# Kernel tuning notes

Hardware: AMD Instinct MI355X
Metric: run time of the kernel (lower is better)

## Reference

```python
import jax, jax.numpy as jnp
import numpy as np

PROJ_DIM = 8192
INPUT_DIM = 512
THRESH = 1e-08


def _signed_sqrt(x):
    return jnp.sign(x) * jnp.sqrt(jnp.abs(x))


def _make_sketch_matrix(key, input_dim, proj_dim):
    kh, ks = jax.random.split(key)
    h = jax.random.randint(kh, (input_dim,), 0, proj_dim)
    s = jnp.sign(jax.random.uniform(ks, (input_dim,), minval=-1.0, maxval=1.0)).astype(jnp.float32)
    M = jnp.zeros((input_dim, proj_dim), dtype=jnp.float32)
    return M.at[jnp.arange(input_dim), h].set(s)


def setup_inputs() -> dict:
    key = jax.random.key(0)
    kx, k1, k2 = jax.random.split(key, 3)
    x = jax.random.normal(kx, (32, 14, 14, INPUT_DIM), dtype=jnp.float32)
    M1 = _make_sketch_matrix(k1, INPUT_DIM, PROJ_DIM)
    M2 = _make_sketch_matrix(k2, INPUT_DIM, PROJ_DIM)
    return {"x": x, "M1": M1, "M2": M2}


def reference(x, M1, M2):
    B, H, W, C = x.shape
    x_flat = x.reshape(-1, C)                      # [B*H*W, C]
    # count-sketch projections (dense matmul, as in the original layer)
    p1 = (x_flat @ M1).astype(jnp.complex64)       # [B*H*W, P]
    p2 = (x_flat @ M2).astype(jnp.complex64)
    # circular convolution via FFT
    sketch = jnp.fft.fft(p1, axis=-1) * jnp.fft.fft(p2, axis=-1)
    y = jnp.real(jnp.fft.ifft(sketch, axis=-1)).astype(jnp.float32)
    y = y.reshape(B, H, W, -1).sum(axis=(1, 2))    # sum-pool over spatial dims -> [B, P]
    y = _signed_sqrt(y)
    # tf.nn.l2_normalize(x, axis=1, epsilon=1e-10)
    inv_norm = jax.lax.rsqrt(jnp.maximum(jnp.sum(y * y, axis=1, keepdims=True), 1e-10))
    return y * inv_norm
```

## Files before the change

### kernel.cpp

```cpp
#include <hip/hip_runtime.h>
#include <math.h>

#define PROJ 8192
#define CDIM 512
#define HWPOS 196
#define NBATCH 32
#define SPLITS 32
#define ROWS_PER_SPLIT (CDIM / SPLITS)

__global__ __launch_bounds__(256) void extract_kernel(
    const float* __restrict__ M1, const float* __restrict__ M2,
    int* __restrict__ h1, float* __restrict__ s1,
    int* __restrict__ h2, float* __restrict__ s2,
    float* __restrict__ norm)
{
    const int row = blockIdx.x;
    const float* M = blockIdx.y ? M2 : M1;
    int*   h = blockIdx.y ? h2 : h1;
    float* s = blockIdx.y ? s2 : s1;
    const float* mrow = M + (size_t)row * PROJ;

    if (blockIdx.x == 0 && blockIdx.y == 0 && threadIdx.x < NBATCH)
        norm[threadIdx.x] = 0.0f;

    for (int i = threadIdx.x * 4; i < PROJ; i += 256 * 4) {
        float4 v = *(const float4*)(mrow + i);
        if (v.x != 0.0f) { h[row] = i + 0; s[row] = v.x; }
        if (v.y != 0.0f) { h[row] = i + 1; s[row] = v.y; }
        if (v.z != 0.0f) { h[row] = i + 2; s[row] = v.z; }
        if (v.w != 0.0f) { h[row] = i + 3; s[row] = v.w; }
    }
}

__global__ __launch_bounds__(256) void gram_kernel(
    const float* __restrict__ x, float* __restrict__ G)
{
    const int bat = blockIdx.z;
    const int bi  = blockIdx.x;
    const int bj  = blockIdx.y;

    __shared__ __align__(16) float As[8][128];
    __shared__ __align__(16) float Bs[8][128];

    const float* Xb = x + (size_t)bat * HWPOS * CDIM;

    float acc[8][8];
#pragma unroll
    for (int i = 0; i < 8; ++i)
#pragma unroll
        for (int j = 0; j < 8; ++j) acc[i][j] = 0.0f;

    const int tid  = threadIdx.x;
    const int ti   = tid >> 4;
    const int tj   = tid & 15;
    const int lrow = tid >> 5;
    const int lcol = (tid & 31) * 4;

    for (int k0 = 0; k0 < HWPOS; k0 += 8) {
        const int krow = k0 + lrow;
        float4 a4 = make_float4(0.f, 0.f, 0.f, 0.f);
        float4 b4 = make_float4(0.f, 0.f, 0.f, 0.f);
        if (krow < HWPOS) {
            const float* xr = Xb + (size_t)krow * CDIM;
            a4 = *(const float4*)(xr + bi * 128 + lcol);
            b4 = *(const float4*)(xr + bj * 128 + lcol);
        }
        *(float4*)&As[lrow][lcol] = a4;
        *(float4*)&Bs[lrow][lcol] = b4;
        __syncthreads();

#pragma unroll
        for (int kk = 0; kk < 8; ++kk) {
            float4 alo = *(const float4*)&As[kk][ti * 8];
            float4 ahi = *(const float4*)&As[kk][ti * 8 + 4];
            float4 blo = *(const float4*)&Bs[kk][tj * 8];
            float4 bhi = *(const float4*)&Bs[kk][tj * 8 + 4];
            float av[8] = {alo.x, alo.y, alo.z, alo.w, ahi.x, ahi.y, ahi.z, ahi.w};
            float bv[8] = {blo.x, blo.y, blo.z, blo.w, bhi.x, bhi.y, bhi.z, bhi.w};
#pragma unroll
            for (int i = 0; i < 8; ++i)
#pragma unroll
                for (int j = 0; j < 8; ++j)
                    acc[i][j] = fmaf(av[i], bv[j], acc[i][j]);
        }
        __syncthreads();
    }

    float* Gb = G + (size_t)bat * CDIM * CDIM;
#pragma unroll
    for (int i = 0; i < 8; ++i) {
        const int row = bi * 128 + ti * 8 + i;
        float* gr = Gb + (size_t)row * CDIM + bj * 128 + tj * 8;
        *(float4*)(gr)     = make_float4(acc[i][0], acc[i][1], acc[i][2], acc[i][3]);
        *(float4*)(gr + 4) = make_float4(acc[i][4], acc[i][5], acc[i][6], acc[i][7]);
    }
}

__global__ __launch_bounds__(256) void scatter_partial_kernel(
    float* __restrict__ G,
    const int* __restrict__ h1, const float* __restrict__ s1,
    const int* __restrict__ h2, const float* __restrict__ s2)
{
    const int spl = blockIdx.x;
    const int bat = blockIdx.y;
    const int tid = threadIdx.x;

    __shared__ float bins[PROJ];
    __shared__ int   sh1[ROWS_PER_SPLIT];
    __shared__ float ss1[ROWS_PER_SPLIT];
    __shared__ int   sh2[CDIM];
    __shared__ float ss2[CDIM];

    for (int i = tid; i < PROJ; i += 256) bins[i] = 0.0f;
    if (tid < ROWS_PER_SPLIT) {
        sh1[tid] = h1[spl * ROWS_PER_SPLIT + tid];
        ss1[tid] = s1[spl * ROWS_PER_SPLIT + tid];
    }
    for (int i = tid; i < CDIM; i += 256) { sh2[i] = h2[i]; ss2[i] = s2[i]; }
    __syncthreads();

    float* Gblk = G + (size_t)bat * CDIM * CDIM + (size_t)spl * ROWS_PER_SPLIT * CDIM;

#pragma unroll
    for (int it = 0; it < 8; ++it) {
        const int p   = it * 1024 + tid * 4;
        const int c1l = p >> 9;
        const int c2  = p & 511;
        float4 g = *(const float4*)(Gblk + p);
        const int   base = sh1[c1l];
        const float sg1  = ss1[c1l];
        atomicAdd(&bins[(base + sh2[c2 + 0]) & (PROJ - 1)], sg1 * ss2[c2 + 0] * g.x);
        atomicAdd(&bins[(base + sh2[c2 + 1]) & (PROJ - 1)], sg1 * ss2[c2 + 1] * g.y);
        atomicAdd(&bins[(base + sh2[c2 + 2]) & (PROJ - 1)], sg1 * ss2[c2 + 2] * g.z);
        atomicAdd(&bins[(base + sh2[c2 + 3]) & (PROJ - 1)], sg1 * ss2[c2 + 3] * g.w);
    }
    __syncthreads();

#pragma unroll
    for (int it = 0; it < 8; ++it) {
        const int i = it * 1024 + tid * 4;
        *(float4*)(Gblk + i) = *(const float4*)&bins[i];
    }
}

__global__ __launch_bounds__(256) void reduce_kernel(
    const float* __restrict__ G, float* __restrict__ out,
    float* __restrict__ norm)
{
    const int chunk = blockIdx.x;
    const int bat   = blockIdx.y;
    const int tid   = threadIdx.x;
    const int base  = chunk * 1024 + tid * 4;

    const float* Gb = G + (size_t)bat * CDIM * CDIM;

    float4 v = make_float4(0.f, 0.f, 0.f, 0.f);
#pragma unroll
    for (int s = 0; s < SPLITS; ++s) {
        float4 p = *(const float4*)(Gb + (size_t)s * PROJ + base);
        v.x += p.x; v.y += p.y; v.z += p.z; v.w += p.w;
    }

    float4 sv;
    sv.x = (v.x >= 0.f) ? sqrtf(v.x) : -sqrtf(-v.x);
    sv.y = (v.y >= 0.f) ? sqrtf(v.y) : -sqrtf(-v.y);
    sv.z = (v.z >= 0.f) ? sqrtf(v.z) : -sqrtf(-v.z);
    sv.w = (v.w >= 0.f) ? sqrtf(v.w) : -sqrtf(-v.w);
    *(float4*)(out + (size_t)bat * PROJ + base) = sv;

    float local = fabsf(v.x) + fabsf(v.y) + fabsf(v.z) + fabsf(v.w);
#pragma unroll
    for (int off = 32; off > 0; off >>= 1) local += __shfl_down(local, off, 64);

    __shared__ float wred[4];
    if ((tid & 63) == 0) wred[tid >> 6] = local;
    __syncthreads();
    if (tid == 0)
        atomicAdd(&norm[bat], wred[0] + wred[1] + wred[2] + wred[3]);
}

__global__ __launch_bounds__(256) void normalize_kernel(
    float* __restrict__ out, const float* __restrict__ norm)
{
    const int bat = blockIdx.y;
    const int idx = blockIdx.x * 1024 + threadIdx.x * 4;
    const float inv = rsqrtf(fmaxf(norm[bat], 1e-10f));
    float4* p = (float4*)(out + (size_t)bat * PROJ + idx);
    float4 v = *p;
    v.x *= inv; v.y *= inv; v.z *= inv; v.w *= inv;
    *p = v;
}

extern "C" void kernel_launch(void* const* d_in, const int* in_sizes, int n_in,
                              void* d_out, int out_size, void* d_ws, size_t ws_size,
                              hipStream_t stream)
{
    const float* x  = (const float*)d_in[0];
    const float* M1 = (const float*)d_in[1];
    const float* M2 = (const float*)d_in[2];
    float* out = (float*)d_out;

    char* ws = (char*)d_ws;
    int*   h1   = (int*)  (ws + 0);
    float* s1   = (float*)(ws + 2048);
    int*   h2   = (int*)  (ws + 4096);
    float* s2   = (float*)(ws + 6144);
    float* norm = (float*)(ws + 8192);
    float* G    = (float*)(ws + 16384);

    extract_kernel<<<dim3(512, 2), 256, 0, stream>>>(M1, M2, h1, s1, h2, s2, norm);
    gram_kernel<<<dim3(4, 4, NBATCH), 256, 0, stream>>>(x, G);
    scatter_partial_kernel<<<dim3(SPLITS, NBATCH), 256, 0, stream>>>(G, h1, s1, h2, s2);
    reduce_kernel<<<dim3(8, NBATCH), 256, 0, stream>>>(G, out, norm);
    normalize_kernel<<<dim3(8, NBATCH), 256, 0, stream>>>(out, norm);
}
```

Measured before the change: 187.6 us.

## Fuse Gram and scatter using split-bf16 MFMA with symmetric tile reuse

A prep kernel now transposes x and converts it to hi/lo bf16 pairs packed in an MFMA-friendly layout. A fused kernel computes each Gram tile with bf16 MFMA using three products (hh, hl, lh) to emulate fp32 accuracy, then scatters straight into shared-memory count-sketch bins. It visits only the 10 upper-triangular tiles and mirrors each off-diagonal contribution. This removes the fp32 FMA Gram, the full 32 MB G round trip through global memory, and half the tile work, at the cost of some precision loss from the split-bf16 emulation and more LDS atomics per tile.

```diff
diff --git a/kernel.cpp b/kernel.cpp
--- a/kernel.cpp
+++ b/kernel.cpp
@@ -5,8 +5,21 @@
 #define CDIM 512
 #define HWPOS 196
 #define NBATCH 32
-#define SPLITS 32
-#define ROWS_PER_SPLIT (CDIM / SPLITS)
+#define KPAD 224
+#define NSLAB 7
+#define NTP 10
+
+typedef __attribute__((ext_vector_type(8))) short   short8;
+typedef __attribute__((ext_vector_type(4))) float   f32x4;
+
+__device__ __forceinline__ unsigned short f2bf(float f) {
+    unsigned u = __float_as_uint(f);
+    u += 0x7fff + ((u >> 16) & 1);
+    return (unsigned short)(u >> 16);
+}
+__device__ __forceinline__ float bf2f(unsigned short h) {
+    return __uint_as_float(((unsigned)h) << 16);
+}
 
 __global__ __launch_bounds__(256) void extract_kernel(
     const float* __restrict__ M1, const float* __restrict__ M2,
@@ -32,119 +45,150 @@
     }
 }
 
-__global__ __launch_bounds__(256) void gram_kernel(
-    const float* __restrict__ x, float* __restrict__ G)
-{
-    const int bat = blockIdx.z;
-    const int bi  = blockIdx.x;
-    const int bj  = blockIdx.y;
-
-    __shared__ __align__(16) float As[8][128];
-    __shared__ __align__(16) float Bs[8][128];
-
-    const float* Xb = x + (size_t)bat * HWPOS * CDIM;
-
-    float acc[8][8];
-#pragma unroll
-    for (int i = 0; i < 8; ++i)
-#pragma unroll
-        for (int j = 0; j < 8; ++j) acc[i][j] = 0.0f;
-
-    const int tid  = threadIdx.x;
-    const int ti   = tid >> 4;
-    const int tj   = tid & 15;
-    const int lrow = tid >> 5;
-    const int lcol = (tid & 31) * 4;
-
-    for (int k0 = 0; k0 < HWPOS; k0 += 8) {
-        const int krow = k0 + lrow;
-        float4 a4 = make_float4(0.f, 0.f, 0.f, 0.f);
-        float4 b4 = make_float4(0.f, 0.f, 0.f, 0.f);
-        if (krow < HWPOS) {
-            const float* xr = Xb + (size_t)krow * CDIM;
-            a4 = *(const float4*)(xr + bi * 128 + lcol);
-            b4 = *(const float4*)(xr + bj * 128 + lcol);
-        }
-        *(float4*)&As[lrow][lcol] = a4;
-        *(float4*)&Bs[lrow][lcol] = b4;
-        __syncthreads();
-
-#pragma unroll
-        for (int kk = 0; kk < 8; ++kk) {
-            float4 alo = *(const float4*)&As[kk][ti * 8];
-            float4 ahi = *(const float4*)&As[kk][ti * 8 + 4];
-            float4 blo = *(const float4*)&Bs[kk][tj * 8];
-            float4 bhi = *(const float4*)&Bs[kk][tj * 8 + 4];
-            float av[8] = {alo.x, alo.y, alo.z, alo.w, ahi.x, ahi.y, ahi.z, ahi.w};
-            float bv[8] = {blo.x, blo.y, blo.z, blo.w, bhi.x, bhi.y, bhi.z, bhi.w};
-#pragma unroll
-            for (int i = 0; i < 8; ++i)
-#pragma unroll
-                for (int j = 0; j < 8; ++j)
-                    acc[i][j] = fmaf(av[i], bv[j], acc[i][j]);
-        }
-        __syncthreads();
-    }
-
-    float* Gb = G + (size_t)bat * CDIM * CDIM;
-#pragma unroll
-    for (int i = 0; i < 8; ++i) {
-        const int row = bi * 128 + ti * 8 + i;
-        float* gr = Gb + (size_t)row * CDIM + bj * 128 + tj * 8;
-        *(float4*)(gr)     = make_float4(acc[i][0], acc[i][1], acc[i][2], acc[i][3]);
-        *(float4*)(gr + 4) = make_float4(acc[i][4], acc[i][5], acc[i][6], acc[i][7]);
-    }
-}
-
-__global__ __launch_bounds__(256) void scatter_partial_kernel(
-    float* __restrict__ G,
-    const int* __restrict__ h1, const float* __restrict__ s1,
-    const int* __restrict__ h2, const float* __restrict__ s2)
-{
-    const int spl = blockIdx.x;
+__global__ __launch_bounds__(256) void prep_kernel(
+    const float* __restrict__ x,
+    unsigned short* __restrict__ XThi, unsigned short* __restrict__ XTlo)
+{
+    const int ks  = blockIdx.x;
     const int bat = blockIdx.y;
     const int tid = threadIdx.x;
-
+    __shared__ float xt[32][513];
+
+    const float* xb = x + (size_t)bat * HWPOS * CDIM;
+    const int k0 = ks * 32;
+#pragma unroll
+    for (int i = 0; i < 16; ++i) {
+        const int idx = i * 1024 + tid * 4;
+        const int kr  = idx >> 9;
+        const int c   = idx & 511;
+        float4 v = make_float4(0.f, 0.f, 0.f, 0.f);
+        if (k0 + kr < HWPOS) v = *(const float4*)(xb + (size_t)(k0 + kr) * CDIM + c);
+        xt[kr][c+0] = v.x; xt[kr][c+1] = v.y; xt[kr][c+2] = v.z; xt[kr][c+3] = v.w;
+    }
+    __syncthreads();
+
+    unsigned short* ohi = XThi + ((size_t)bat * NSLAB + ks) * 16384;
+    unsigned short* olo = XTlo + ((size_t)bat * NSLAB + ks) * 16384;
+#pragma unroll
+    for (int i = 0; i < 8; ++i) {
+        const int ch   = i * 256 + tid;
+        const int c16  = ch & 15;
+        const int quad = (ch >> 4) & 3;
+        const int cgrp = ch >> 6;
+        const int c    = cgrp * 16 + c16;
+        short8 vh, vl;
+#pragma unroll
+        for (int j = 0; j < 8; ++j) {
+            float f = xt[quad * 8 + j][c];
+            unsigned short h = f2bf(f);
+            vh[j] = (short)h;
+            vl[j] = (short)f2bf(f - bf2f(h));
+        }
+        *(short8*)(ohi + ch * 8) = vh;
+        *(short8*)(olo + ch * 8) = vl;
+    }
+}
+
+__global__ __launch_bounds__(256) void gramscatter_kernel(
+    const unsigned short* __restrict__ XThi, const unsigned short* __restrict__ XTlo,
+    const int* __restrict__ h1, const float* __restrict__ s1,
+    const int* __restrict__ h2, const float* __restrict__ s2,
+    float* __restrict__ pbins)
+{
+    const int tp  = blockIdx.x;
+    const int bat = blockIdx.y;
+    const int bi  = (tp < 4) ? 0 : (tp < 7) ? 1 : (tp < 9) ? 2 : 3;
+    const int bj  = (tp < 4) ? tp : (tp < 7) ? (tp - 3) : (tp < 9) ? (tp - 5) : 3;
+    const int tid  = threadIdx.x;
+    const int w    = tid >> 6;
+    const int lane = tid & 63;
+
+    __shared__ __align__(16) unsigned short Sbuf[4][4096];
     __shared__ float bins[PROJ];
-    __shared__ int   sh1[ROWS_PER_SPLIT];
-    __shared__ float ss1[ROWS_PER_SPLIT];
-    __shared__ int   sh2[CDIM];
-    __shared__ float ss2[CDIM];
-
-    for (int i = tid; i < PROJ; i += 256) bins[i] = 0.0f;
-    if (tid < ROWS_PER_SPLIT) {
-        sh1[tid] = h1[spl * ROWS_PER_SPLIT + tid];
-        ss1[tid] = s1[spl * ROWS_PER_SPLIT + tid];
-    }
-    for (int i = tid; i < CDIM; i += 256) { sh2[i] = h2[i]; ss2[i] = s2[i]; }
-    __syncthreads();
-
-    float* Gblk = G + (size_t)bat * CDIM * CDIM + (size_t)spl * ROWS_PER_SPLIT * CDIM;
-
-#pragma unroll
-    for (int it = 0; it < 8; ++it) {
-        const int p   = it * 1024 + tid * 4;
-        const int c1l = p >> 9;
-        const int c2  = p & 511;
-        float4 g = *(const float4*)(Gblk + p);
-        const int   base = sh1[c1l];
-        const float sg1  = ss1[c1l];
-        atomicAdd(&bins[(base + sh2[c2 + 0]) & (PROJ - 1)], sg1 * ss2[c2 + 0] * g.x);
-        atomicAdd(&bins[(base + sh2[c2 + 1]) & (PROJ - 1)], sg1 * ss2[c2 + 1] * g.y);
-        atomicAdd(&bins[(base + sh2[c2 + 2]) & (PROJ - 1)], sg1 * ss2[c2 + 2] * g.z);
-        atomicAdd(&bins[(base + sh2[c2 + 3]) & (PROJ - 1)], sg1 * ss2[c2 + 3] * g.w);
-    }
-    __syncthreads();
-
-#pragma unroll
-    for (int it = 0; it < 8; ++it) {
-        const int i = it * 1024 + tid * 4;
-        *(float4*)(Gblk + i) = *(const float4*)&bins[i];
-    }
+    __shared__ int   th1[256]; __shared__ float ts1[256];
+    __shared__ int   th2[256]; __shared__ float ts2[256];
+
+    for (int i = tid; i < PROJ; i += 256) bins[i] = 0.f;
+    {
+        const int g = (tid < 128) ? (bi * 128 + tid) : (bj * 128 + tid - 128);
+        th1[tid] = h1[g]; ts1[tid] = s1[g];
+        th2[tid] = h2[g]; ts2[tid] = s2[g];
+    }
+
+    const int tile = (w < 2) ? bi : bj;
+    const unsigned short* srcbase = ((w & 1) ? XTlo : XThi)
+                                  + (size_t)bat * NSLAB * 16384 + (size_t)tile * 4096;
+    const int rowq = w >> 1, colq = w & 1;
+
+    f32x4 acc[16];
+#pragma unroll
+    for (int i = 0; i < 16; ++i) { acc[i][0]=0.f; acc[i][1]=0.f; acc[i][2]=0.f; acc[i][3]=0.f; }
+
+    __syncthreads();
+
+    for (int ks = 0; ks < NSLAB; ++ks) {
+        const unsigned short* src = srcbase + (size_t)ks * 16384;
+#pragma unroll
+        for (int i = 0; i < 8; ++i) {
+            const int off = i * 512 + lane * 8;
+            *(short8*)&Sbuf[w][off] = *(const short8*)(src + off);
+        }
+        __syncthreads();
+
+        short8 ah[4], al[4], bh[4], bl[4];
+#pragma unroll
+        for (int t = 0; t < 4; ++t) {
+            ah[t] = *(const short8*)&Sbuf[0][(rowq * 4 + t) * 512 + lane * 8];
+            al[t] = *(const short8*)&Sbuf[1][(rowq * 4 + t) * 512 + lane * 8];
+            bh[t] = *(const short8*)&Sbuf[2][(colq * 4 + t) * 512 + lane * 8];
+            bl[t] = *(const short8*)&Sbuf[3][(colq * 4 + t) * 512 + lane * 8];
+        }
+#pragma unroll
+        for (int mt = 0; mt < 4; ++mt)
+#pragma unroll
+            for (int nt = 0; nt < 4; ++nt) {
+                const int idx = mt * 4 + nt;
+                acc[idx] = __builtin_amdgcn_mfma_f32_16x16x32_bf16(ah[mt], bh[nt], acc[idx], 0, 0, 0);
+                acc[idx] = __builtin_amdgcn_mfma_f32_16x16x32_bf16(ah[mt], bl[nt], acc[idx], 0, 0, 0);
+                acc[idx] = __builtin_amdgcn_mfma_f32_16x16x32_bf16(al[mt], bh[nt], acc[idx], 0, 0, 0);
+            }
+        __syncthreads();
+    }
+
+    const bool mirror = (bi != bj);
+    int   h2c[4], h1c[4];
+    float s2c[4], s1c[4];
+#pragma unroll
+    for (int nt = 0; nt < 4; ++nt) {
+        const int cl = colq * 64 + nt * 16 + (lane & 15);
+        h2c[nt] = th2[128 + cl]; s2c[nt] = ts2[128 + cl];
+        h1c[nt] = th1[128 + cl]; s1c[nt] = ts1[128 + cl];
+    }
+    const int quad = lane >> 4;
+#pragma unroll
+    for (int mt = 0; mt < 4; ++mt)
+#pragma unroll
+        for (int reg = 0; reg < 4; ++reg) {
+            const int rl = rowq * 64 + mt * 16 + quad * 4 + reg;
+            const int   h1r = th1[rl]; const float s1r = ts1[rl];
+            const int   h2r = th2[rl]; const float s2r = ts2[rl];
+#pragma unroll
+            for (int nt = 0; nt < 4; ++nt) {
+                const float v = acc[mt * 4 + nt][reg];
+                atomicAdd(&bins[(h1r + h2c[nt]) & (PROJ - 1)], s1r * s2c[nt] * v);
+                if (mirror)
+                    atomicAdd(&bins[(h1c[nt] + h2r) & (PROJ - 1)], s1c[nt] * s2r * v);
+            }
+        }
+    __syncthreads();
+
+    float* dst = pbins + ((size_t)bat * NTP + tp) * PROJ;
+    for (int i = tid * 4; i < PROJ; i += 1024)
+        *(float4*)(dst + i) = *(const float4*)&bins[i];
 }
 
 __global__ __launch_bounds__(256) void reduce_kernel(
-    const float* __restrict__ G, float* __restrict__ out,
+    const float* __restrict__ pbins, float* __restrict__ out,
     float* __restrict__ norm)
 {
     const int chunk = blockIdx.x;
@@ -152,12 +196,11 @@
     const int tid   = threadIdx.x;
     const int base  = chunk * 1024 + tid * 4;
 
-    const float* Gb = G + (size_t)bat * CDIM * CDIM;
-
+    const float* pb = pbins + (size_t)bat * NTP * PROJ;
     float4 v = make_float4(0.f, 0.f, 0.f, 0.f);
 #pragma unroll
-    for (int s = 0; s < SPLITS; ++s) {
-        float4 p = *(const float4*)(Gb + (size_t)s * PROJ + base);
+    for (int t = 0; t < NTP; ++t) {
+        float4 p = *(const float4*)(pb + (size_t)t * PROJ + base);
         v.x += p.x; v.y += p.y; v.z += p.z; v.w += p.w;
     }
 
@@ -201,16 +244,18 @@
     float* out = (float*)d_out;
 
     char* ws = (char*)d_ws;
-    int*   h1   = (int*)  (ws + 0);
-    float* s1   = (float*)(ws + 2048);
-    int*   h2   = (int*)  (ws + 4096);
-    float* s2   = (float*)(ws + 6144);
-    float* norm = (float*)(ws + 8192);
-    float* G    = (float*)(ws + 16384);
+    int*            h1    = (int*)   (ws + 0);
+    float*          s1    = (float*) (ws + 2048);
+    int*            h2    = (int*)   (ws + 4096);
+    float*          s2    = (float*) (ws + 6144);
+    float*          norm  = (float*) (ws + 8192);
+    unsigned short* XThi  = (unsigned short*)(ws + 16384);
+    unsigned short* XTlo  = (unsigned short*)(ws + 7356416);
+    float*          pbins = (float*) (ws + 14696448);
 
     extract_kernel<<<dim3(512, 2), 256, 0, stream>>>(M1, M2, h1, s1, h2, s2, norm);
-    gram_kernel<<<dim3(4, 4, NBATCH), 256, 0, stream>>>(x, G);
-    scatter_partial_kernel<<<dim3(SPLITS, NBATCH), 256, 0, stream>>>(G, h1, s1, h2, s2);
-    reduce_kernel<<<dim3(8, NBATCH), 256, 0, stream>>>(G, out, norm);
+    prep_kernel<<<dim3(NSLAB, NBATCH), 256, 0, stream>>>(x, XThi, XTlo);
+    gramscatter_kernel<<<dim3(NTP, NBATCH), 256, 0, stream>>>(XThi, XTlo, h1, s1, h2, s2, pbins);
+    reduce_kernel<<<dim3(8, NBATCH), 256, 0, stream>>>(pbins, out, norm);
     normalize_kernel<<<dim3(8, NBATCH), 256, 0, stream>>>(out, norm);
 }
```

After: 195.0 us. 3.9% more time.
